# Kernel tuning notes

Measured on AMD Instinct MI355X. Metric: run time of the kernel, lower is better.

Reference implementation:

```python
import jax, jax.numpy as jnp
import numpy as np
import math

B, S, H, NH = 2, 2048, 1024, 16
DK = H // NH


def setup_inputs() -> dict:
    key = jax.random.key(0)
    k1, k2, k3 = jax.random.split(key, 3)
    scale = 1.0 / math.sqrt(H)
    return {
        "x": jax.random.normal(k1, (B, S, H), dtype=jnp.float32),
        "w_attn": jax.random.normal(k2, (H, 3 * H), dtype=jnp.float32) * scale,
        "b_attn": jnp.zeros((3 * H,), dtype=jnp.float32),
        "w_proj": jax.random.normal(k3, (H, H), dtype=jnp.float32) * scale,
        "b_proj": jnp.zeros((H,), dtype=jnp.float32),
    }


def reference(x, w_attn, b_attn, w_proj, b_proj):
    bs, seq_len, hidden = x.shape
    qkv = x @ w_attn + b_attn                       # [B,S,3H]
    q, k, v = jnp.split(qkv, 3, axis=-1)
    # [B,S,H] -> [B,NH,S,DK]
    def heads(t):
        return t.reshape(bs, seq_len, NH, DK).transpose(0, 2, 1, 3)
    q, k, v = heads(q), heads(k), heads(v)
    scores = jnp.einsum('bhqd,bhkd->bhqk', q, k) / math.sqrt(DK)  # [B,NH,S,S]
    causal = jnp.tril(jnp.ones((seq_len, seq_len), dtype=bool))
    scores = jnp.where(causal[None, None], scores, -jnp.inf)
    attn = jax.nn.softmax(scores, axis=-1)
    out = jnp.einsum('bhqk,bhkd->bhqd', attn, v)    # [B,NH,S,DK]
    out = out.transpose(0, 2, 1, 3).reshape(bs, seq_len, hidden)
    return out @ w_proj + b_proj
```

## Files before the change

kernel.cpp:

```cpp
#include <hip/hip_runtime.h>

#define BATCH 2
#define S_LEN 2048
#define NHEADS 16
#define DKV 64
#define HID 1024

typedef __attribute__((ext_vector_type(8))) short s16x8;
typedef __attribute__((ext_vector_type(4))) short s16x4;
typedef __attribute__((ext_vector_type(4))) float f32x4;

__device__ inline unsigned short f2bf(float f) {
    union { float f; unsigned int u; } v; v.f = f;
    unsigned int r = v.u + 0x7fffu + ((v.u >> 16) & 1u);
    return (unsigned short)(r >> 16);
}

__device__ inline s16x8 pack8(float4 a, float4 b) {
    s16x8 r;
    r[0] = (short)f2bf(a.x); r[1] = (short)f2bf(a.y);
    r[2] = (short)f2bf(a.z); r[3] = (short)f2bf(a.w);
    r[4] = (short)f2bf(b.x); r[5] = (short)f2bf(b.y);
    r[6] = (short)f2bf(b.z); r[7] = (short)f2bf(b.w);
    return r;
}

__device__ inline void gload_lds16(const void* g, void* l) {
    __builtin_amdgcn_global_load_lds(
        (const __attribute__((address_space(1))) void*)g,
        (__attribute__((address_space(3))) void*)l, 16, 0, 0);
}

__device__ inline unsigned int cvtpk_bf16(float lo, float hi) {
    unsigned int d;
    asm("v_cvt_pk_bf16_f32 %0, %1, %2" : "=v"(d) : "v"(lo), "v"(hi));
    return d;
}

__global__ __launch_bounds__(256)
void f32_to_bf16_kernel(const float* __restrict__ in, unsigned short* __restrict__ out, int n8) {
    int i = blockIdx.x * 256 + threadIdx.x;
    if (i < n8) {
        const float4* p = (const float4*)(in + (size_t)i * 8);
        float4 a = p[0], b = p[1];
        *(s16x8*)(out + (size_t)i * 8) = pack8(a, b);
    }
}

__global__ __launch_bounds__(256)
void transpose_bf16_kernel(const float* __restrict__ in, unsigned short* __restrict__ out,
                           int K, int N) {
    __shared__ float tile[32][33];
    int n0 = blockIdx.x * 32;
    int k0 = blockIdx.y * 32;
    int tx = threadIdx.x, ty = threadIdx.y;
    for (int i = ty; i < 32; i += 8)
        tile[i][tx] = in[(size_t)(k0 + i) * N + n0 + tx];
    __syncthreads();
    for (int i = ty; i < 32; i += 8)
        out[(size_t)(n0 + i) * K + k0 + tx] = f2bf(tile[tx][i]);
}

__global__ __launch_bounds__(256)
void gemm_qkv_kernel(const unsigned short* __restrict__ A, const unsigned short* __restrict__ Bt,
                     const float* __restrict__ bias, unsigned short* __restrict__ qkv,
                     unsigned short* __restrict__ vT, int M, int N, int K) {
    __shared__ __align__(16) unsigned short As[128 * 64];
    __shared__ __align__(16) unsigned short Bs[128 * 64];

    const int tid  = threadIdx.x;
    const int lane = tid & 63;
    const int wv   = tid >> 6;
    const int wr   = wv >> 1, wc = wv & 1;
    const int m0   = blockIdx.y * 128, n0 = blockIdx.x * 128;

    const int lr = lane & 15;
    const int lg = lane >> 4;

    const int srow = lane >> 3;
    const int scol = ((lane & 7) ^ srow) * 8;

    f32x4 acc[4][4] = {};

    for (int k0 = 0; k0 < K; k0 += 64) {
        __syncthreads();
        #pragma unroll
        for (int l = 0; l < 4; l++) {
            const int r0 = wv * 32 + l * 8;
            gload_lds16(A  + (size_t)(m0 + r0 + srow) * K + k0 + scol, &As[r0 * 64]);
            gload_lds16(Bt + (size_t)(n0 + r0 + srow) * K + k0 + scol, &Bs[r0 * 64]);
        }
        __syncthreads();

        #pragma unroll
        for (int kk = 0; kk < 2; kk++) {
            s16x8 af[4], bfr[4];
            #pragma unroll
            for (int mi = 0; mi < 4; mi++)
                af[mi] = *(const s16x8*)&As[(wr * 64 + mi * 16 + lr) * 64 + (((kk * 4 + lg) ^ (lr & 7)) * 8)];
            #pragma unroll
            for (int ni = 0; ni < 4; ni++)
                bfr[ni] = *(const s16x8*)&Bs[(wc * 64 + ni * 16 + lr) * 64 + (((kk * 4 + lg) ^ (lr & 7)) * 8)];
            #pragma unroll
            for (int mi = 0; mi < 4; mi++)
                #pragma unroll
                for (int ni = 0; ni < 4; ni++)
                    acc[mi][ni] = __builtin_amdgcn_mfma_f32_16x16x32_bf16(af[mi], bfr[ni], acc[mi][ni], 0, 0, 0);
        }
    }

    const bool isV = (n0 >= 2 * HID);
    #pragma unroll
    for (int mi = 0; mi < 4; mi++) {
        #pragma unroll
        for (int ni = 0; ni < 4; ni++) {
            int col = n0 + wc * 64 + ni * 16 + lr;
            float bv = bias[col];
            int row0 = m0 + wr * 64 + mi * 16 + lg * 4;
            if (isV) {
                int d = col - 2 * HID;
                int bb = row0 >> 11;
                int s = row0 & (S_LEN - 1);
                int sl = s & 63;
                int sp = (sl & 0x23) | ((sl & 0x10) >> 2) | ((sl & 0x0C) << 1);
                int sc = (s & ~63) | sp;
                s16x4 pk;
                #pragma unroll
                for (int r = 0; r < 4; r++)
                    pk[r] = (short)f2bf(acc[mi][ni][r] + bv);
                *(s16x4*)&vT[((size_t)bb * HID + d) * S_LEN + sc] = pk;
            } else {
                #pragma unroll
                for (int r = 0; r < 4; r++)
                    qkv[(size_t)(row0 + r) * N + col] = f2bf(acc[mi][ni][r] + bv);
            }
        }
    }
}

__global__ __launch_bounds__(256)
void gemm64_kernel(const unsigned short* __restrict__ A, const unsigned short* __restrict__ Bt,
                   const float* __restrict__ bias, float* __restrict__ Cout,
                   int M, int N, int K) {
    __shared__ __align__(16) unsigned short As[64 * 32];
    __shared__ __align__(16) unsigned short Bs[128 * 32];

    const int tid  = threadIdx.x;
    const int lane = tid & 63;
    const int wv   = tid >> 6;
    const int wr   = wv >> 1, wc = wv & 1;
    const int m0   = blockIdx.y * 64, n0 = blockIdx.x * 128;

    const int lr = lane & 15;
    const int lg = lane >> 4;
    const int lk = lg * 8;

    const int srow = lane >> 2;
    const int scol = (lane & 3) * 8;

    const int arow = tid >> 2;
    const int acol = (tid & 3) * 8;

    f32x4 acc[2][4] = {};

    for (int k0 = 0; k0 < K; k0 += 32) {
        __syncthreads();
        gload_lds16(A + (size_t)(m0 + arow) * K + k0 + acol, &As[(arow & ~3) * 32]);
        #pragma unroll
        for (int l = 0; l < 2; l++) {
            const int r0 = wv * 32 + l * 16;
            gload_lds16(Bt + (size_t)(n0 + r0 + srow) * K + k0 + scol, &Bs[r0 * 32]);
        }
        __syncthreads();

        s16x8 af[2], bfr[4];
        #pragma unroll
        for (int mi = 0; mi < 2; mi++)
            af[mi] = *(const s16x8*)&As[(wr * 32 + mi * 16 + lr) * 32 + lk];
        #pragma unroll
        for (int ni = 0; ni < 4; ni++)
            bfr[ni] = *(const s16x8*)&Bs[(wc * 64 + ni * 16 + lr) * 32 + lk];
        #pragma unroll
        for (int mi = 0; mi < 2; mi++)
            #pragma unroll
            for (int ni = 0; ni < 4; ni++)
                acc[mi][ni] = __builtin_amdgcn_mfma_f32_16x16x32_bf16(af[mi], bfr[ni], acc[mi][ni], 0, 0, 0);
    }

    #pragma unroll
    for (int mi = 0; mi < 2; mi++) {
        #pragma unroll
        for (int ni = 0; ni < 4; ni++) {
            int col = n0 + wc * 64 + ni * 16 + lr;
            float bv = bias[col];
            #pragma unroll
            for (int r = 0; r < 4; r++) {
                int row = m0 + wr * 32 + mi * 16 + lg * 4 + r;
                Cout[(size_t)row * N + col] = acc[mi][ni][r] + bv;
            }
        }
    }
}

__global__ __launch_bounds__(256)
void attn_kernel(const unsigned short* __restrict__ qkv, const unsigned short* __restrict__ vT,
                 unsigned short* __restrict__ out) {
    __shared__ __align__(16) unsigned short Ks[2][64 * 64];
    __shared__ __align__(16) unsigned short Vs[2][64 * 64];

    const int tid  = threadIdx.x;
    const int lane = tid & 63;
    const int w    = tid >> 6;

    const int wgid = blockIdx.x;
    const int xcd  = wgid & 7;
    const int slot = wgid >> 3;
    const int pp   = slot & 15;
    const int g    = (slot >> 4) * 8 + xcd;
    const int head = g & 15;
    const int b    = g >> 4;

    const size_t rowbase = (size_t)b * S_LEN;
    const int hoff = head * DKV;

    const int lr = lane & 15;
    const int lg = lane >> 4;
    const int lk = lg * 8;

    const int krow   = lane >> 3;
    const int kchunk = ((lane & 7) ^ krow) * 8;

    #pragma unroll
    for (int panel = 0; panel < 2; panel++) {
        const int qb = (panel == 0) ? pp : (31 - pp);
        const int q0 = qb * 64;
        const int nt = qb + 1;

        s16x8 qf[2];
        {
            const unsigned short* qp = qkv + (rowbase + q0 + w * 16 + lr) * (3 * HID) + hoff;
            qf[0] = *(const s16x8*)(qp + lk);
            qf[1] = *(const s16x8*)(qp + 32 + lk);
        }

        f32x4 o[4] = {};
        float lsum = 0.0f;
        int cur = 0;

        __syncthreads();
        #pragma unroll
        for (int l = 0; l < 2; l++) {
            const int r0 = (w * 2 + l) * 8;
            gload_lds16(qkv + (rowbase + r0 + krow) * (3 * HID) + HID + hoff + kchunk,
                        &Ks[0][r0 * 64]);
            gload_lds16(vT + ((size_t)b * HID + hoff + r0 + krow) * S_LEN + kchunk,
                        &Vs[0][r0 * 64]);
        }

        for (int tt = 0; tt < nt; tt++) {
            __syncthreads();

            if (tt + 1 < nt) {
                const int jn = (tt + 1) * 64;
                #pragma unroll
                for (int l = 0; l < 2; l++) {
                    const int r0 = (w * 2 + l) * 8;
                    gload_lds16(qkv + (rowbase + jn + r0 + krow) * (3 * HID) + HID + hoff + kchunk,
                                &Ks[cur ^ 1][r0 * 64]);
                    gload_lds16(vT + ((size_t)b * HID + hoff + r0 + krow) * S_LEN + jn + kchunk,
                                &Vs[cur ^ 1][r0 * 64]);
                }
            }

            f32x4 sfT[4] = {};
            #pragma unroll
            for (int kt = 0; kt < 2; kt++)
                #pragma unroll
                for (int ni = 0; ni < 4; ni++) {
                    s16x8 kb = *(const s16x8*)&Ks[cur][(ni * 16 + lr) * 64 + (((kt * 4 + lg) ^ (lr & 7)) * 8)];
                    sfT[ni] = __builtin_amdgcn_mfma_f32_16x16x32_bf16(kb, qf[kt], sfT[ni], 0, 0, 0);
                }

            const bool diag = (tt == nt - 1);
            unsigned int own[4][2];
            #pragma unroll
            for (int ni = 0; ni < 4; ni++) {
                float pv[4];
                #pragma unroll
                for (int r = 0; r < 4; r++) {
                    float s = sfT[ni][r];
                    if (diag) {
                        int kl = ni * 16 + lg * 4 + r;
                        if (kl > w * 16 + lr) s = -INFINITY;
                    }
                    pv[r] = exp2f(__fmaf_rn(s, 0.18033688f, -17.3123405f));
                }
                lsum += (pv[0] + pv[1]) + (pv[2] + pv[3]);
                own[ni][0] = cvtpk_bf16(pv[0], pv[1]);
                own[ni][1] = cvtpk_bf16(pv[2], pv[3]);
            }

            #pragma unroll
            for (int kt = 0; kt < 2; kt++) {
                union { unsigned int u[4]; s16x8 v; } pa;
                pa.u[0] = own[2 * kt][0];
                pa.u[1] = own[2 * kt][1];
                pa.u[2] = own[2 * kt + 1][0];
                pa.u[3] = own[2 * kt + 1][1];
                #pragma unroll
                for (int dt = 0; dt < 4; dt++) {
                    s16x8 vb = *(const s16x8*)&Vs[cur][(dt * 16 + lr) * 64 + (((kt * 4 + lg) ^ (lr & 7)) * 8)];
                    o[dt] = __builtin_amdgcn_mfma_f32_16x16x32_bf16(vb, pa.v, o[dt], 0, 0, 0);
                }
            }
            cur ^= 1;
        }

        lsum += __shfl_xor(lsum, 16, 64);
        lsum += __shfl_xor(lsum, 32, 64);
        float invl = 1.0f / lsum;
        int qrow = q0 + w * 16 + lr;
        #pragma unroll
        for (int dt = 0; dt < 4; dt++) {
            s16x4 pk;
            #pragma unroll
            for (int r = 0; r < 4; r++) pk[r] = (short)f2bf(o[dt][r] * invl);
            *(s16x4*)&out[(rowbase + qrow) * HID + hoff + dt * 16 + lg * 4] = pk;
        }
    }
}

extern "C" void kernel_launch(void* const* d_in, const int* in_sizes, int n_in,
                              void* d_out, int out_size, void* d_ws, size_t ws_size,
                              hipStream_t stream) {
    const float* x      = (const float*)d_in[0];
    const float* w_attn = (const float*)d_in[1];
    const float* b_attn = (const float*)d_in[2];
    const float* w_proj = (const float*)d_in[3];
    const float* b_proj = (const float*)d_in[4];
    float* out = (float*)d_out;

    char* ws = (char*)d_ws;
    unsigned short* qkv      = (unsigned short*)(ws);
    unsigned short* waT      = (unsigned short*)(ws + 25165824);
    unsigned short* wpT      = (unsigned short*)(ws + 31457280);
    unsigned short* attn_out = (unsigned short*)(ws + 33554432);
    unsigned short* xb       = (unsigned short*)(ws + 41943040);
    unsigned short* vTr      = (unsigned short*)(ws + 50331648);

    const int M = BATCH * S_LEN;

    f32_to_bf16_kernel<<<dim3((M * HID / 8 + 255) / 256), 256, 0, stream>>>(x, xb, M * HID / 8);

    dim3 tb(32, 8);
    transpose_bf16_kernel<<<dim3(3 * HID / 32, HID / 32), tb, 0, stream>>>(w_attn, waT, HID, 3 * HID);
    transpose_bf16_kernel<<<dim3(HID / 32, HID / 32), tb, 0, stream>>>(w_proj, wpT, HID, HID);

    gemm_qkv_kernel<<<dim3(3 * HID / 128, M / 128), 256, 0, stream>>>(
        xb, waT, b_attn, qkv, vTr, M, 3 * HID, HID);

    attn_kernel<<<dim3(512), 256, 0, stream>>>(qkv, vTr, attn_out);

    gemm64_kernel<<<dim3(HID / 128, M / 64), 256, 0, stream>>>(
        attn_out, wpT, b_proj, out, M, HID, HID);
}
```

Measured before the change: 124.3 us.

## Double-buffer LDS tiles in QKV and projection GEMMs to overlap loads with MFMA

Both GEMM kernels now keep two LDS buffers. They prefetch the next K-slice with async global-to-LDS loads while the current slice feeds the MFMAs, and they drop one barrier per iteration. The QKV GEMM's K-tile also shrinks from 64 to 32 to keep shared memory the same size, and this removes its XOR bank swizzle. The aim is to hide global memory latency behind compute. The risks are LDS bank conflicts in the unswizzled layout and more loop iterations with fewer MFMAs between barriers.

Result: no change. 121.9 us (-1.9%).

```diff
diff --git a/kernel.cpp b/kernel.cpp
--- a/kernel.cpp
+++ b/kernel.cpp
@@ -65,8 +65,8 @@
 void gemm_qkv_kernel(const unsigned short* __restrict__ A, const unsigned short* __restrict__ Bt,
                      const float* __restrict__ bias, unsigned short* __restrict__ qkv,
                      unsigned short* __restrict__ vT, int M, int N, int K) {
-    __shared__ __align__(16) unsigned short As[128 * 64];
-    __shared__ __align__(16) unsigned short Bs[128 * 64];
+    __shared__ __align__(16) unsigned short As[2][128 * 32];
+    __shared__ __align__(16) unsigned short Bs[2][128 * 32];
 
     const int tid  = threadIdx.x;
     const int lane = tid & 63;
@@ -76,37 +76,46 @@
 
     const int lr = lane & 15;
     const int lg = lane >> 4;
-
-    const int srow = lane >> 3;
-    const int scol = ((lane & 7) ^ srow) * 8;
+    const int lk = lg * 8;
+
+    const int srow = lane >> 2;
+    const int scol = (lane & 3) * 8;
 
     f32x4 acc[4][4] = {};
-
-    for (int k0 = 0; k0 < K; k0 += 64) {
+    int cur = 0;
+
+    #pragma unroll
+    for (int l = 0; l < 2; l++) {
+        const int r0 = wv * 32 + l * 16;
+        gload_lds16(A  + (size_t)(m0 + r0 + srow) * K + scol, &As[0][r0 * 32]);
+        gload_lds16(Bt + (size_t)(n0 + r0 + srow) * K + scol, &Bs[0][r0 * 32]);
+    }
+
+    for (int k0 = 0; k0 < K; k0 += 32) {
         __syncthreads();
-        #pragma unroll
-        for (int l = 0; l < 4; l++) {
-            const int r0 = wv * 32 + l * 8;
-            gload_lds16(A  + (size_t)(m0 + r0 + srow) * K + k0 + scol, &As[r0 * 64]);
-            gload_lds16(Bt + (size_t)(n0 + r0 + srow) * K + k0 + scol, &Bs[r0 * 64]);
-        }
-        __syncthreads();
-
-        #pragma unroll
-        for (int kk = 0; kk < 2; kk++) {
-            s16x8 af[4], bfr[4];
-            #pragma unroll
-            for (int mi = 0; mi < 4; mi++)
-                af[mi] = *(const s16x8*)&As[(wr * 64 + mi * 16 + lr) * 64 + (((kk * 4 + lg) ^ (lr & 7)) * 8)];
+
+        if (k0 + 32 < K) {
+            #pragma unroll
+            for (int l = 0; l < 2; l++) {
+                const int r0 = wv * 32 + l * 16;
+                gload_lds16(A  + (size_t)(m0 + r0 + srow) * K + k0 + 32 + scol, &As[cur ^ 1][r0 * 32]);
+                gload_lds16(Bt + (size_t)(n0 + r0 + srow) * K + k0 + 32 + scol, &Bs[cur ^ 1][r0 * 32]);
+            }
+        }
+
+        s16x8 af[4], bfr[4];
+        #pragma unroll
+        for (int mi = 0; mi < 4; mi++)
+            af[mi] = *(const s16x8*)&As[cur][(wr * 64 + mi * 16 + lr) * 32 + lk];
+        #pragma unroll
+        for (int ni = 0; ni < 4; ni++)
+            bfr[ni] = *(const s16x8*)&Bs[cur][(wc * 64 + ni * 16 + lr) * 32 + lk];
+        #pragma unroll
+        for (int mi = 0; mi < 4; mi++)
             #pragma unroll
             for (int ni = 0; ni < 4; ni++)
-                bfr[ni] = *(const s16x8*)&Bs[(wc * 64 + ni * 16 + lr) * 64 + (((kk * 4 + lg) ^ (lr & 7)) * 8)];
-            #pragma unroll
-            for (int mi = 0; mi < 4; mi++)
-                #pragma unroll
-                for (int ni = 0; ni < 4; ni++)
-                    acc[mi][ni] = __builtin_amdgcn_mfma_f32_16x16x32_bf16(af[mi], bfr[ni], acc[mi][ni], 0, 0, 0);
-        }
+                acc[mi][ni] = __builtin_amdgcn_mfma_f32_16x16x32_bf16(af[mi], bfr[ni], acc[mi][ni], 0, 0, 0);
+        cur ^= 1;
     }
 
     const bool isV = (n0 >= 2 * HID);
@@ -142,8 +151,8 @@
 void gemm64_kernel(const unsigned short* __restrict__ A, const unsigned short* __restrict__ Bt,
                    const float* __restrict__ bias, float* __restrict__ Cout,
                    int M, int N, int K) {
-    __shared__ __align__(16) unsigned short As[64 * 32];
-    __shared__ __align__(16) unsigned short Bs[128 * 32];
+    __shared__ __align__(16) unsigned short As[2][64 * 32];
+    __shared__ __align__(16) unsigned short Bs[2][128 * 32];
 
     const int tid  = threadIdx.x;
     const int lane = tid & 63;
@@ -162,29 +171,40 @@
     const int acol = (tid & 3) * 8;
 
     f32x4 acc[2][4] = {};
+    int cur = 0;
+
+    gload_lds16(A + (size_t)(m0 + arow) * K + acol, &As[0][(arow & ~3) * 32]);
+    #pragma unroll
+    for (int l = 0; l < 2; l++) {
+        const int r0 = wv * 32 + l * 16;
+        gload_lds16(Bt + (size_t)(n0 + r0 + srow) * K + scol, &Bs[0][r0 * 32]);
+    }
 
     for (int k0 = 0; k0 < K; k0 += 32) {
         __syncthreads();
-        gload_lds16(A + (size_t)(m0 + arow) * K + k0 + acol, &As[(arow & ~3) * 32]);
-        #pragma unroll
-        for (int l = 0; l < 2; l++) {
-            const int r0 = wv * 32 + l * 16;
-            gload_lds16(Bt + (size_t)(n0 + r0 + srow) * K + k0 + scol, &Bs[r0 * 32]);
-        }
-        __syncthreads();
+
+        if (k0 + 32 < K) {
+            gload_lds16(A + (size_t)(m0 + arow) * K + k0 + 32 + acol, &As[cur ^ 1][(arow & ~3) * 32]);
+            #pragma unroll
+            for (int l = 0; l < 2; l++) {
+                const int r0 = wv * 32 + l * 16;
+                gload_lds16(Bt + (size_t)(n0 + r0 + srow) * K + k0 + 32 + scol, &Bs[cur ^ 1][r0 * 32]);
+            }
+        }
 
         s16x8 af[2], bfr[4];
         #pragma unroll
         for (int mi = 0; mi < 2; mi++)
-            af[mi] = *(const s16x8*)&As[(wr * 32 + mi * 16 + lr) * 32 + lk];
+            af[mi] = *(const s16x8*)&As[cur][(wr * 32 + mi * 16 + lr) * 32 + lk];
         #pragma unroll
         for (int ni = 0; ni < 4; ni++)
-            bfr[ni] = *(const s16x8*)&Bs[(wc * 64 + ni * 16 + lr) * 32 + lk];
+            bfr[ni] = *(const s16x8*)&Bs[cur][(wc * 64 + ni * 16 + lr) * 32 + lk];
         #pragma unroll
         for (int mi = 0; mi < 2; mi++)
             #pragma unroll
             for (int ni = 0; ni < 4; ni++)
                 acc[mi][ni] = __builtin_amdgcn_mfma_f32_16x16x32_bf16(af[mi], bfr[ni], acc[mi][ni], 0, 0, 0);
+        cur ^= 1;
     }
 
     #pragma unroll
```
